# Kernel tuning notes

Measured on AMD Instinct MI355X. Metric: run time of the kernel, lower is better.

Reference implementation:

```python
import jax, jax.numpy as jnp
import numpy as np
import math

H, C, PQ, PV = 12, 16, 4, 8  # heads, head dim, query points, value points
C_S, C_Z = 384, 128
W_C = math.sqrt(2.0 / (9.0 * PQ))
W_L = math.sqrt(1.0 / 3.0)


def setup_inputs() -> dict:
    key = jax.random.key(0)
    ks = jax.random.split(key, 14)
    B, N = 1, 768
    s = jax.random.normal(ks[0], (B, N, C_S), dtype=jnp.float32)
    z = jax.random.normal(ks[1], (B, N, N, C_Z), dtype=jnp.float32)
    R = jax.random.normal(ks[2], (B, N, 3, 3), dtype=jnp.float32)
    t = jax.random.normal(ks[3], (B, N, 3), dtype=jnp.float32)

    def lin(k, fan_in, fan_out):
        return jax.random.normal(k, (fan_in, fan_out), dtype=jnp.float32) / math.sqrt(fan_in)

    out_in = H * C + H * PV * 3 + H * C_Z  # 2016
    return {
        "single_representation": s,
        "pair_representation": z,
        "rotations": R,
        "translation": t,
        "W_q": lin(ks[4], C_S, H * C),
        "W_k": lin(ks[5], C_S, H * C),
        "W_v": lin(ks[6], C_S, H * C),
        "W_qp": lin(ks[7], C_S, 3 * H * PQ),
        "W_kp": lin(ks[8], C_S, 3 * H * PQ),
        "W_vp": lin(ks[9], C_S, 3 * H * PV),
        "W_b": lin(ks[10], C_Z, H),
        "W_out": lin(ks[11], out_in, C_S),
        "b_out": jnp.zeros((C_S,), dtype=jnp.float32),
    }


def reference(single_representation, pair_representation, rotations, translation,
              W_q, W_k, W_v, W_qp, W_kp, W_vp, W_b, W_out, b_out):
    s, z, R, t = single_representation, pair_representation, rotations, translation
    B, N, _ = s.shape

    # scalar q/k/v: [B,N,H,C]
    q = (s @ W_q).reshape(B, N, H, C)
    k = (s @ W_k).reshape(B, N, H, C)
    v = (s @ W_v).reshape(B, N, H, C)

    # local points -> global frames: x_glob = R x_loc + t
    def to_global(pts_flat, P):
        pts = pts_flat.reshape(B, N, H, P, 3)
        return jnp.einsum('bnij,bnhpj->bnhpi', R, pts) + t[:, :, None, None, :]

    q_pts = to_global(s @ W_qp, PQ)  # [B,N,H,PQ,3]
    k_pts = to_global(s @ W_kp, PQ)
    v_pts = to_global(s @ W_vp, PV)  # [B,N,H,PV,3]

    # scalar attention term
    qk = jnp.einsum('bnhc,bmhc->bhnm', q, k) / math.sqrt(C)
    # pair bias term
    bias = jnp.einsum('bnmz,zh->bhnm', z, W_b)
    # point distance term: sum_p ||q_i - k_j||^2 expanded to avoid [N,N,H,P,3]
    qn = jnp.sum(q_pts * q_pts, axis=(-2, -1))  # [B,N,H]
    kn = jnp.sum(k_pts * k_pts, axis=(-2, -1))
    cross = jnp.einsum('bnhpx,bmhpx->bhnm', q_pts, k_pts)
    sq_dist = qn.transpose(0, 2, 1)[:, :, :, None] + kn.transpose(0, 2, 1)[:, :, None, :] - 2.0 * cross

    logits = W_L * (qk + bias - 0.5 * W_C * sq_dist)  # [B,H,N,M]
    a = jax.nn.softmax(logits, axis=-1)

    # outputs
    o = jnp.einsum('bhnm,bmhc->bnhc', a, v).reshape(B, N, H * C)
    o_pts_g = jnp.einsum('bhnm,bmhpx->bnhpx', a, v_pts)
    # inverse frame: R^T (x - t)
    o_pts = jnp.einsum('bnij,bnhpi->bnhpj', R, o_pts_g - t[:, :, None, None, :])
    o_pts = o_pts.reshape(B, N, H * PV * 3)
    o_pair = jnp.einsum('bhnm,bnmz->bnhz', a, z).reshape(B, N, H * C_Z)

    cat = jnp.concatenate([o, o_pts, o_pair], axis=-1)  # [B,N,2016]
    return cat @ W_out + b_out  # [B,N,c_s]
```

## Files before the change

kernel.cpp:

```cpp
#include <hip/hip_runtime.h>
#include <math.h>

#define RAW_OFF   0u
#define QPTS_OFF  884736u
#define KPTS_OFF  995328u
#define VPTS_OFF  1105920u
#define QN_OFF    1327104u
#define KN_OFF    1336320u
#define CAT_OFF   1345536u
#define QP_OFF    2893824u
#define KP_OFF    3041280u
#define SLOG_OFF  3188736u
#define PART2_OFF 10266624u
#define WT_OFF    14118912u

#define WL 0.5773502691896258f
#define WC 0.23570226039551587f
#define CKN (-0.5f*WL*WC)

typedef __attribute__((ext_vector_type(8))) short short8;
typedef __attribute__((ext_vector_type(4))) float f32x4;

__device__ __forceinline__ unsigned short f2bf1(float a) {
  unsigned u = __builtin_bit_cast(unsigned, a);
  return (unsigned short)((u + 0x7fff + ((u >> 16) & 1)) >> 16);
}
__device__ __forceinline__ unsigned f2bf2(float a, float b) {
  unsigned ua = __builtin_bit_cast(unsigned, a), ub = __builtin_bit_cast(unsigned, b);
  return (unsigned)((ua + 0x7fff + ((ua >> 16) & 1)) >> 16)
       | ((ub + 0x7fff + ((ub >> 16) & 1)) & 0xffff0000u);
}
__device__ __forceinline__ float bf2f(unsigned short u) {
  return __builtin_bit_cast(float, ((unsigned)u) << 16);
}

#define BAR_LDS() asm volatile("s_waitcnt lgkmcnt(0)\n\ts_barrier" ::: "memory")

__global__ __launch_bounds__(256) void wcvt(
    const float* __restrict__ Wout, unsigned short* __restrict__ WT)
{
  __shared__ float tl[32][33];
  int b = blockIdx.x;
  int kt = b % 63, ct = b / 63;
  int k0 = kt*32, c0 = ct*32;
  int tr = threadIdx.x >> 5, tc = threadIdx.x & 31;
  #pragma unroll
  for (int i = 0; i < 4; ++i)
    tl[tr + i*8][tc] = Wout[(size_t)(k0 + tr + i*8)*384 + c0 + tc];
  __syncthreads();
  #pragma unroll
  for (int i = 0; i < 4; ++i) {
    int c = tr + i*8;
    WT[(size_t)(c0 + c)*2016 + k0 + tc] = f2bf1(tl[tc][c]);
  }
}

__global__ __launch_bounds__(256) void prep_gemm(
    const float* __restrict__ s, const float* __restrict__ Wq, const float* __restrict__ Wk,
    const float* __restrict__ Wv, const float* __restrict__ Wqp, const float* __restrict__ Wkp,
    const float* __restrict__ Wvp, float* __restrict__ raw)
{
  int t = threadIdx.x;
  int bc = blockIdx.x % 24, br = blockIdx.x / 24;
  int row0 = br * 32, cb = bc * 48;
  const float* W; int outdim, c0;
  if (cb < 192)      { W = Wq;  outdim = 192; c0 = cb; }
  else if (cb < 384) { W = Wk;  outdim = 192; c0 = cb - 192; }
  else if (cb < 576) { W = Wv;  outdim = 192; c0 = cb - 384; }
  else if (cb < 720) { W = Wqp; outdim = 144; c0 = cb - 576; }
  else if (cb < 864) { W = Wkp; outdim = 144; c0 = cb - 720; }
  else               { W = Wvp; outdim = 288; c0 = cb - 864; }

  __shared__ float s_l[32*33];
  __shared__ float w_l[32*49];
  float acc[2][3] = {};
  int tr = t >> 4, tc = t & 15;

  for (int k0 = 0; k0 < 384; k0 += 32) {
    #pragma unroll
    for (int i = 0; i < 4; ++i) {
      int idx = i*256 + t, r = idx >> 5, kk = idx & 31;
      s_l[r*33 + kk] = s[(row0 + r)*384 + k0 + kk];
    }
    #pragma unroll
    for (int i = 0; i < 6; ++i) {
      int idx = i*256 + t, kk = idx / 48, c = idx % 48;
      w_l[kk*49 + c] = W[(k0 + kk)*outdim + c0 + c];
    }
    __syncthreads();
    #pragma unroll
    for (int kk = 0; kk < 32; ++kk) {
      float a0 = s_l[(tr*2+0)*33 + kk], a1 = s_l[(tr*2+1)*33 + kk];
      float b0 = w_l[kk*49 + tc*3 + 0], b1 = w_l[kk*49 + tc*3 + 1], b2 = w_l[kk*49 + tc*3 + 2];
      acc[0][0] += a0*b0; acc[0][1] += a0*b1; acc[0][2] += a0*b2;
      acc[1][0] += a1*b0; acc[1][1] += a1*b1; acc[1][2] += a1*b2;
    }
    __syncthreads();
  }
  #pragma unroll
  for (int i = 0; i < 2; ++i)
    #pragma unroll
    for (int j = 0; j < 3; ++j)
      raw[(row0 + tr*2 + i)*1152 + cb + tc*3 + j] = acc[i][j];
}

__global__ __launch_bounds__(256) void transform_pts(
    const float* __restrict__ raw, const float* __restrict__ R, const float* __restrict__ tg,
    float* __restrict__ qpts, float* __restrict__ kpts, float* __restrict__ vpts,
    float* __restrict__ qn, float* __restrict__ kn)
{
  int n = blockIdx.x, t = threadIdx.x;
  __shared__ float tl[576];
  const float* R9 = R + n*9;
  const float* tv = tg + n*3;
  for (int i = 0; i < 3; ++i) {
    int j = i*256 + t;
    if (j >= 576) break;
    int jj, basecol; float* dst; int dstoff;
    if (j < 144)      { jj = j;      basecol = 576; dst = qpts; dstoff = n*144 + jj; }
    else if (j < 288) { jj = j-144;  basecol = 720; dst = kpts; dstoff = n*144 + jj; }
    else              { jj = j-288;  basecol = 864; dst = vpts; dstoff = n*288 + jj; }
    int x = jj % 3;
    const float* p = raw + n*1152 + basecol + (jj - x);
    float val = R9[x*3+0]*p[0] + R9[x*3+1]*p[1] + R9[x*3+2]*p[2] + tv[x];
    dst[dstoff] = val;
    tl[j] = val;
  }
  __syncthreads();
  if (t < 24) {
    int side = t / 12, h = t % 12;
    const float* q = tl + side*144 + h*12;
    float sm = 0.f;
    #pragma unroll
    for (int r = 0; r < 12; ++r) sm += q[r]*q[r];
    (side == 0 ? qn : kn)[n*12 + h] = sm;
  }
}

__global__ __launch_bounds__(384) void qkprep(
    const float* __restrict__ raw, const float* __restrict__ qpts,
    const float* __restrict__ kpts, short* __restrict__ Qp, short* __restrict__ Kp)
{
  int n = blockIdx.x, t = threadIdx.x;
  int h = t >> 5, k = t & 31;
  float qv, kv;
  if (k < 16)      { qv = (WL*0.25f) * raw[n*1152 + h*16 + k];       kv = raw[n*1152 + 192 + h*16 + k]; }
  else if (k < 28) { qv = (WL*WC) * qpts[n*144 + h*12 + (k-16)];     kv = kpts[n*144 + h*12 + (k-16)]; }
  else             { qv = 0.f; kv = 0.f; }
  Qp[n*384 + t] = (short)f2bf1(qv);
  Kp[n*384 + t] = (short)f2bf1(kv);
}

__global__ __launch_bounds__(512) void logits_gemm(
    const short* __restrict__ Qp, const short* __restrict__ Kp,
    const float* __restrict__ kn, float* __restrict__ slog)
{
  int t = threadIdx.x, b = blockIdx.x;
  int bn = b / 12, bm = b % 12;
  int lane = t & 63, wid = t >> 6;
  int nsub = wid & 3, msub = wid >> 2;
  int l15 = lane & 15, kg = lane >> 4;
  int nrow = bn*64 + nsub*16 + l15;
  int mbase = bm*64 + msub*32;

  f32x4 acc[2][12];
  #pragma unroll
  for (int mt = 0; mt < 2; ++mt)
    #pragma unroll
    for (int h = 0; h < 12; ++h) acc[mt][h] = (f32x4){0.f,0.f,0.f,0.f};

  #pragma unroll
  for (int h = 0; h < 12; ++h) {
    short8 af = *(const short8*)(Qp + (size_t)(nrow*12 + h)*32 + kg*8);
    #pragma unroll
    for (int mt = 0; mt < 2; ++mt) {
      int m = mbase + mt*16 + l15;
      short8 bf = *(const short8*)(Kp + (size_t)(m*12 + h)*32 + kg*8);
      acc[mt][h] = __builtin_amdgcn_mfma_f32_16x16x32_bf16(af, bf, acc[mt][h], 0, 0, 0);
    }
  }
  #pragma unroll
  for (int mt = 0; mt < 2; ++mt) {
    int m = mbase + mt*16 + l15;
    float knadj[12];
    #pragma unroll
    for (int h = 0; h < 12; ++h) knadj[h] = CKN * kn[m*12 + h];
    #pragma unroll
    for (int r = 0; r < 4; ++r) {
      int nr = bn*64 + nsub*16 + kg*4 + r;
      size_t base = ((size_t)nr*768 + m)*12;
      #pragma unroll
      for (int hq = 0; hq < 3; ++hq) {
        float4 v;
        v.x = acc[mt][hq*4+0][r] + knadj[hq*4+0];
        v.y = acc[mt][hq*4+1][r] + knadj[hq*4+1];
        v.z = acc[mt][hq*4+2][r] + knadj[hq*4+2];
        v.w = acc[mt][hq*4+3][r] + knadj[hq*4+3];
        *(float4*)(slog + base + hq*4) = v;
      }
    }
  }
}

#define Z_L   0
#define BIASL 4352
#define PT    5440
#define S_L   6016
#define SMEMW 6028

__global__ __launch_bounds__(256, 2) void ipa_main(
    const float* __restrict__ z, const float* __restrict__ raw,
    const float* __restrict__ slog, const float* __restrict__ vpts,
    const float* __restrict__ Wb, float* __restrict__ part2)
{
  __shared__ __align__(16) unsigned smem[SMEMW];
  float* smf = (float*)smem;
  unsigned short* lds16 = (unsigned short*)smem;
  int bx = blockIdx.x;
  int n = bx >> 1, hb = bx & 1;
  int t = threadIdx.x;
  int lane = t & 63, wid = t >> 6;
  int l15 = lane & 15, kg = lane >> 4;

  if (t < 12) smf[S_L + t] = 0.f;

  short8 wbf[4];
  {
    #pragma unroll
    for (int ks = 0; ks < 4; ++ks)
      #pragma unroll
      for (int e = 0; e < 8; ++e) {
        int kk = ks*32 + kg*8 + e;
        float v = (l15 < 12) ? WL * Wb[kk*12 + l15] : 0.f;
        wbf[ks][e] = (short)f2bf1(v);
      }
  }

  f32x4 oacc[2];
  oacc[0] = (f32x4){0.f,0.f,0.f,0.f};
  oacc[1] = (f32x4){0.f,0.f,0.f,0.f};

  bool dact = t < 240;
  int mh = t / 120, slot = t % 120;
  const float* dsrc; int dstride, dh;
  if (slot < 48) { dh = slot >> 2;     dsrc = raw + 384 + slot*4;  dstride = 1152; }
  else           { dh = (slot-48) / 6; dsrc = vpts + (slot-48)*4;  dstride = 288;  }
  float da0 = 0.f, da1 = 0.f, da2 = 0.f, da3 = 0.f;

  const float* zrow = z + (size_t)n*768*128;
  int ssm = t >> 5, ssc = t & 31;

  float4 zst[8];
  #define STAGE_LOAD(M0)                                                     \
    _Pragma("unroll")                                                        \
    for (int i = 0; i < 8; ++i)                                              \
      zst[i] = *(const float4*)(zrow + (size_t)((M0) + i*8 + ssm)*128 + ssc*4);
  #define STAGE_WRITE()                                                      \
    _Pragma("unroll")                                                        \
    for (int i = 0; i < 8; ++i) {                                            \
      unsigned w0 = f2bf2(zst[i].x, zst[i].y);                               \
      unsigned w1 = f2bf2(zst[i].z, zst[i].w);                               \
      uint2 uu; uu.x = w0; uu.y = w1;                                        \
      *(uint2*)&smem[Z_L + (i*8 + ssm)*68 + ssc*2] = uu;                     \
    }

  const size_t slb = (size_t)n * 9216 + (size_t)hb * 4608;
  float4 sl, slnext;

  STAGE_LOAD(hb*384);
  if (t < 192) sl = *(const float4*)(slog + slb + t*4);
  STAGE_WRITE();
  BAR_LDS();

  for (int it = 0; it < 6; ++it) {
    int m0 = hb*384 + it*64;
    if (it < 5) {
      STAGE_LOAD(m0 + 64);
      if (t < 192) slnext = *(const float4*)(slog + slb + (size_t)(it+1)*768 + t*4);
    }

    {
      f32x4 bacc = (f32x4){0.f,0.f,0.f,0.f};
      int zbase = (wid*16 + l15)*68;
      #pragma unroll
      for (int ks = 0; ks < 4; ++ks) {
        short8 za = *(const short8*)&smem[Z_L + zbase + kg*4 + ks*16];
        bacc = __builtin_amdgcn_mfma_f32_16x16x32_bf16(za, wbf[ks], bacc, 0, 0, 0);
      }
      #pragma unroll
      for (int r = 0; r < 4; ++r)
        smf[BIASL + (wid*16 + kg*4 + r)*17 + l15] = bacc[r];
    }
    BAR_LDS();

    if (t < 192) {
      float slv[4] = {sl.x, sl.y, sl.z, sl.w};
      #pragma unroll
      for (int e = 0; e < 4; ++e) {
        int ge = t*4 + e;
        int m = ge / 12, h = ge - m*12;
        float p = __expf(slv[e] + smf[BIASL + m*17 + h]);
        lds16[PT*2 + h*72 + m] = f2bf1(p);
      }
    }
    BAR_LDS();

    if (t < 48) {
      int h = t >> 2, seg = t & 3;
      short8 a0 = *(const short8*)&lds16[PT*2 + h*72 + seg*16];
      short8 a1 = *(const short8*)&lds16[PT*2 + h*72 + seg*16 + 8];
      float ps = 0.f;
      #pragma unroll
      for (int e = 0; e < 8; ++e)
        ps += bf2f((unsigned short)a0[e]) + bf2f((unsigned short)a1[e]);
      ps += __shfl_xor(ps, 1);
      ps += __shfl_xor(ps, 2);
      if (seg == 0) smf[S_L + h] += ps;
    }

    {
      short8 af[2];
      #pragma unroll
      for (int ks = 0; ks < 2; ++ks)
        af[ks] = *(const short8*)&lds16[PT*2 + l15*72 + ks*32 + kg*8];
      #pragma unroll
      for (int tt = 0; tt < 2; ++tt) {
        int zc = (wid*2 + tt)*16 + l15;
        #pragma unroll
        for (int ks = 0; ks < 2; ++ks) {
          short8 bf;
          #pragma unroll
          for (int e = 0; e < 8; ++e)
            bf[e] = (short)lds16[Z_L*2 + (ks*32 + kg*8 + e)*136 + zc];
          oacc[tt] = __builtin_amdgcn_mfma_f32_16x16x32_bf16(af[ks], bf, oacc[tt], 0, 0, 0);
        }
      }
    }

    if (dact) {
      #pragma unroll
      for (int j4 = 0; j4 < 4; ++j4) {
        short8 pw = *(const short8*)&lds16[PT*2 + dh*72 + mh*32 + j4*8];
        #pragma unroll
        for (int e = 0; e < 8; ++e) {
          float wq = bf2f((unsigned short)pw[e]);
          int row = m0 + mh*32 + j4*8 + e;
          float4 v = *(const float4*)(dsrc + (size_t)row*dstride);
          da0 += wq*v.x; da1 += wq*v.y; da2 += wq*v.z; da3 += wq*v.w;
        }
      }
    }

    if (it < 5) {
      BAR_LDS();
      STAGE_WRITE();
      if (t < 192) sl = slnext;
    }
    BAR_LDS();
  }

  float* pb = part2 + (size_t)bx * 2508;
  if (t < 12) pb[t] = smf[S_L + t];
  if (dact) {
    float4 dv; dv.x = da0; dv.y = da1; dv.z = da2; dv.w = da3;
    *(float4*)(pb + 12 + (mh*120 + slot)*4) = dv;
  }
  if (kg < 3) {
    #pragma unroll
    for (int tt = 0; tt < 2; ++tt) {
      int zc = (wid*2 + tt)*16 + l15;
      #pragma unroll
      for (int r = 0; r < 4; ++r)
        pb[972 + (kg*4 + r)*128 + zc] = oacc[tt][r];
    }
  }
}

__global__ __launch_bounds__(256) void combine(
    const float* __restrict__ part2, const float* __restrict__ Rg,
    const float* __restrict__ tg, unsigned short* __restrict__ catb)
{
  int n = blockIdx.x, t = threadIdx.x;
  const float* b0 = part2 + (size_t)n*2*2508;
  const float* b1 = b0 + 2508;
  __shared__ float S[12], ogl[288];
  if (t < 12) S[t] = b0[t] + b1[t];
  __syncthreads();
  unsigned short* cb = catb + (size_t)n*2016;
  for (int i = t; i < 480; i += 256) {
    float v = b0[12+i] + b0[12+480+i] + b1[12+i] + b1[12+480+i];
    int slot = i >> 2;
    int dh = (slot < 48) ? (slot >> 2) : ((slot - 48) / 6);
    float val = v / S[dh];
    if (i < 192) cb[i] = f2bf1(val);
    else         ogl[i - 192] = val;
  }
  __syncthreads();
  const float* R9 = Rg + n*9;
  const float* tv = tg + n*3;
  for (int j = t; j < 288; j += 256) {
    int x = j % 3, base = j - x;
    float g0 = ogl[base+0] - tv[0];
    float g1 = ogl[base+1] - tv[1];
    float g2 = ogl[base+2] - tv[2];
    cb[192 + j] = f2bf1(R9[x]*g0 + R9[3+x]*g1 + R9[6+x]*g2);
  }
  for (int e = t; e < 1536; e += 256) {
    int h = e >> 7;
    cb[480 + e] = f2bf1((b0[972+e] + b1[972+e]) / S[h]);
  }
}

__global__ __launch_bounds__(256) void final_mfma(
    const unsigned short* __restrict__ catb, const unsigned short* __restrict__ WT,
    const float* __restrict__ bout, float* __restrict__ out)
{
  int t = threadIdx.x, b = blockIdx.x;
  int rt = b / 6, ct = b % 6;
  int r0 = rt*64, c0 = ct*64;
  int lane = t & 63, wid = t >> 6;
  int l15 = lane & 15, kg = lane >> 4;

  f32x4 acc[4];
  #pragma unroll
  for (int cs = 0; cs < 4; ++cs) acc[cs] = (f32x4){0.f,0.f,0.f,0.f};

  const unsigned short* arow = catb + (size_t)(r0 + wid*16 + l15)*2016;
  for (int k0 = 0; k0 < 2016; k0 += 32) {
    short8 af = *(const short8*)(arow + k0 + kg*8);
    #pragma unroll
    for (int cs = 0; cs < 4; ++cs) {
      short8 bf = *(const short8*)(WT + (size_t)(c0 + cs*16 + l15)*2016 + k0 + kg*8);
      acc[cs] = __builtin_amdgcn_mfma_f32_16x16x32_bf16(af, bf, acc[cs], 0, 0, 0);
    }
  }
  #pragma unroll
  for (int cs = 0; cs < 4; ++cs) {
    #pragma unroll
    for (int r = 0; r < 4; ++r) {
      int nn = r0 + wid*16 + kg*4 + r;
      int c  = c0 + cs*16 + l15;
      out[(size_t)nn*384 + c] = acc[cs][r] + bout[c];
    }
  }
}

extern "C" void kernel_launch(void* const* d_in, const int* in_sizes, int n_in,
                              void* d_out, int out_size, void* d_ws, size_t ws_size,
                              hipStream_t stream) {
  const float* s    = (const float*)d_in[0];
  const float* z    = (const float*)d_in[1];
  const float* R    = (const float*)d_in[2];
  const float* tv   = (const float*)d_in[3];
  const float* Wq   = (const float*)d_in[4];
  const float* Wk   = (const float*)d_in[5];
  const float* Wv   = (const float*)d_in[6];
  const float* Wqp  = (const float*)d_in[7];
  const float* Wkp  = (const float*)d_in[8];
  const float* Wvp  = (const float*)d_in[9];
  const float* Wb   = (const float*)d_in[10];
  const float* Wout = (const float*)d_in[11];
  const float* bout = (const float*)d_in[12];
  float* out = (float*)d_out;
  float* ws  = (float*)d_ws;

  float* raw  = ws + RAW_OFF;
  float* qpts = ws + QPTS_OFF;
  float* kpts = ws + KPTS_OFF;
  float* vpts = ws + VPTS_OFF;
  float* qn   = ws + QN_OFF;
  float* kn   = ws + KN_OFF;
  unsigned short* catb = (unsigned short*)(ws + CAT_OFF);
  short* Qp   = (short*)(ws + QP_OFF);
  short* Kp   = (short*)(ws + KP_OFF);
  float* slog = ws + SLOG_OFF;
  float* part2 = ws + PART2_OFF;
  unsigned short* WT = (unsigned short*)(ws + WT_OFF);

  wcvt<<<756, 256, 0, stream>>>(Wout, WT);
  prep_gemm<<<576, 256, 0, stream>>>(s, Wq, Wk, Wv, Wqp, Wkp, Wvp, raw);
  transform_pts<<<768, 256, 0, stream>>>(raw, R, tv, qpts, kpts, vpts, qn, kn);
  qkprep<<<768, 384, 0, stream>>>(raw, qpts, kpts, Qp, Kp);
  logits_gemm<<<144, 512, 0, stream>>>(Qp, Kp, kn, slog);
  ipa_main<<<1536, 256, 0, stream>>>(z, raw, slog, vpts, Wb, part2);
  combine<<<768, 256, 0, stream>>>(part2, R, tv, catb);
  final_mfma<<<72, 256, 0, stream>>>(catb, WT, bout, out);
}
```

Before: 220.0 us.

## Use bf16 MFMA for input projections and fuse point transform with QK packing

Replaces the fp32 LDS-tiled projection GEMM with a bf16 MFMA kernel, fed by new kernels that convert s and the concatenated, transposed projection weights to bf16. The point transform and QK packing kernels are merged, so query and key points and qn no longer go through global memory. This targets the cost of the scalar fp32 GEMM and one kernel launch. It adds two conversion launches and lowers the precision of the projections, which also affects v and the value points.

```diff
diff --git a/kernel.cpp b/kernel.cpp
--- a/kernel.cpp
+++ b/kernel.cpp
@@ -1,18 +1,17 @@
 #include <hip/hip_runtime.h>
 #include <math.h>
 
-#define RAW_OFF   0u
-#define QPTS_OFF  884736u
-#define KPTS_OFF  995328u
-#define VPTS_OFF  1105920u
-#define QN_OFF    1327104u
-#define KN_OFF    1336320u
-#define CAT_OFF   1345536u
-#define QP_OFF    2893824u
-#define KP_OFF    3041280u
-#define SLOG_OFF  3188736u
-#define PART2_OFF 10266624u
-#define WT_OFF    14118912u
+#define RAW_OFF    0u
+#define VPTS_OFF   884736u
+#define KN_OFF     1105920u
+#define CAT_OFF    1115136u
+#define QP_OFF     1889280u
+#define KP_OFF     2036736u
+#define SLOG_OFF   2184192u
+#define PART2_OFF  9262080u
+#define WT_OFF     13114368u
+#define SB_OFF     13501440u
+#define WTC_OFF    13648896u
 
 #define WL 0.5773502691896258f
 #define WC 0.23570226039551587f
@@ -35,6 +34,37 @@
 }
 
 #define BAR_LDS() asm volatile("s_waitcnt lgkmcnt(0)\n\ts_barrier" ::: "memory")
+
+__global__ __launch_bounds__(256) void scvt(
+    const float* __restrict__ s, unsigned short* __restrict__ sb)
+{
+  int g = blockIdx.x*256 + threadIdx.x;
+  float4 v = *(const float4*)(s + (size_t)g*4);
+  uint2 p; p.x = f2bf2(v.x, v.y); p.y = f2bf2(v.z, v.w);
+  *(uint2*)(sb + (size_t)g*4) = p;
+}
+
+__global__ __launch_bounds__(256) void wcatcvt(
+    const float* __restrict__ Wq, const float* __restrict__ Wk, const float* __restrict__ Wv,
+    const float* __restrict__ Wqp, const float* __restrict__ Wkp, const float* __restrict__ Wvp,
+    unsigned short* __restrict__ wtc)
+{
+  int g = blockIdx.x*256 + threadIdx.x;
+  int c = g / 96, kq = (g % 96) * 4;
+  const float* W; int od, cl;
+  if (c < 192)      { W = Wq;  od = 192; cl = c; }
+  else if (c < 384) { W = Wk;  od = 192; cl = c - 192; }
+  else if (c < 576) { W = Wv;  od = 192; cl = c - 384; }
+  else if (c < 720) { W = Wqp; od = 144; cl = c - 576; }
+  else if (c < 864) { W = Wkp; od = 144; cl = c - 720; }
+  else              { W = Wvp; od = 288; cl = c - 864; }
+  float a = W[(size_t)(kq+0)*od + cl];
+  float b = W[(size_t)(kq+1)*od + cl];
+  float d = W[(size_t)(kq+2)*od + cl];
+  float e = W[(size_t)(kq+3)*od + cl];
+  uint2 p; p.x = f2bf2(a, b); p.y = f2bf2(d, e);
+  *(uint2*)(wtc + (size_t)c*384 + kq) = p;
+}
 
 __global__ __launch_bounds__(256) void wcvt(
     const float* __restrict__ Wout, unsigned short* __restrict__ WT)
@@ -55,100 +85,78 @@
   }
 }
 
-__global__ __launch_bounds__(256) void prep_gemm(
-    const float* __restrict__ s, const float* __restrict__ Wq, const float* __restrict__ Wk,
-    const float* __restrict__ Wv, const float* __restrict__ Wqp, const float* __restrict__ Wkp,
-    const float* __restrict__ Wvp, float* __restrict__ raw)
-{
-  int t = threadIdx.x;
-  int bc = blockIdx.x % 24, br = blockIdx.x / 24;
-  int row0 = br * 32, cb = bc * 48;
-  const float* W; int outdim, c0;
-  if (cb < 192)      { W = Wq;  outdim = 192; c0 = cb; }
-  else if (cb < 384) { W = Wk;  outdim = 192; c0 = cb - 192; }
-  else if (cb < 576) { W = Wv;  outdim = 192; c0 = cb - 384; }
-  else if (cb < 720) { W = Wqp; outdim = 144; c0 = cb - 576; }
-  else if (cb < 864) { W = Wkp; outdim = 144; c0 = cb - 720; }
-  else               { W = Wvp; outdim = 288; c0 = cb - 864; }
-
-  __shared__ float s_l[32*33];
-  __shared__ float w_l[32*49];
-  float acc[2][3] = {};
-  int tr = t >> 4, tc = t & 15;
+__global__ __launch_bounds__(256) void prep_mfma(
+    const unsigned short* __restrict__ sb, const unsigned short* __restrict__ wtc,
+    float* __restrict__ raw)
+{
+  int t = threadIdx.x, b = blockIdx.x;
+  int ct = b % 18, rt = b / 18;
+  int lane = t & 63, wid = t >> 6;
+  int l15 = lane & 15, kg = lane >> 4;
+  int r0 = rt*64 + wid*16, c0 = ct*64;
+
+  f32x4 acc[4];
+  #pragma unroll
+  for (int cs = 0; cs < 4; ++cs) acc[cs] = (f32x4){0.f,0.f,0.f,0.f};
 
   for (int k0 = 0; k0 < 384; k0 += 32) {
-    #pragma unroll
-    for (int i = 0; i < 4; ++i) {
-      int idx = i*256 + t, r = idx >> 5, kk = idx & 31;
-      s_l[r*33 + kk] = s[(row0 + r)*384 + k0 + kk];
-    }
-    #pragma unroll
-    for (int i = 0; i < 6; ++i) {
-      int idx = i*256 + t, kk = idx / 48, c = idx % 48;
-      w_l[kk*49 + c] = W[(k0 + kk)*outdim + c0 + c];
-    }
-    __syncthreads();
-    #pragma unroll
-    for (int kk = 0; kk < 32; ++kk) {
-      float a0 = s_l[(tr*2+0)*33 + kk], a1 = s_l[(tr*2+1)*33 + kk];
-      float b0 = w_l[kk*49 + tc*3 + 0], b1 = w_l[kk*49 + tc*3 + 1], b2 = w_l[kk*49 + tc*3 + 2];
-      acc[0][0] += a0*b0; acc[0][1] += a0*b1; acc[0][2] += a0*b2;
-      acc[1][0] += a1*b0; acc[1][1] += a1*b1; acc[1][2] += a1*b2;
-    }
-    __syncthreads();
-  }
-  #pragma unroll
-  for (int i = 0; i < 2; ++i)
-    #pragma unroll
-    for (int j = 0; j < 3; ++j)
-      raw[(row0 + tr*2 + i)*1152 + cb + tc*3 + j] = acc[i][j];
-}
-
-__global__ __launch_bounds__(256) void transform_pts(
+    short8 af = *(const short8*)(sb + (size_t)(r0 + l15)*384 + k0 + kg*8);
+    #pragma unroll
+    for (int cs = 0; cs < 4; ++cs) {
+      short8 bf = *(const short8*)(wtc + (size_t)(c0 + cs*16 + l15)*384 + k0 + kg*8);
+      acc[cs] = __builtin_amdgcn_mfma_f32_16x16x32_bf16(af, bf, acc[cs], 0, 0, 0);
+    }
+  }
+  #pragma unroll
+  for (int cs = 0; cs < 4; ++cs)
+    #pragma unroll
+    for (int r = 0; r < 4; ++r)
+      raw[(size_t)(r0 + kg*4 + r)*1152 + c0 + cs*16 + l15] = acc[cs][r];
+}
+
+__global__ __launch_bounds__(256) void transform_qk(
     const float* __restrict__ raw, const float* __restrict__ R, const float* __restrict__ tg,
-    float* __restrict__ qpts, float* __restrict__ kpts, float* __restrict__ vpts,
-    float* __restrict__ qn, float* __restrict__ kn)
+    float* __restrict__ vpts, float* __restrict__ kn,
+    short* __restrict__ Qp, short* __restrict__ Kp)
 {
   int n = blockIdx.x, t = threadIdx.x;
   __shared__ float tl[576];
   const float* R9 = R + n*9;
   const float* tv = tg + n*3;
+  #pragma unroll
   for (int i = 0; i < 3; ++i) {
     int j = i*256 + t;
     if (j >= 576) break;
-    int jj, basecol; float* dst; int dstoff;
-    if (j < 144)      { jj = j;      basecol = 576; dst = qpts; dstoff = n*144 + jj; }
-    else if (j < 288) { jj = j-144;  basecol = 720; dst = kpts; dstoff = n*144 + jj; }
-    else              { jj = j-288;  basecol = 864; dst = vpts; dstoff = n*288 + jj; }
+    int jj, basecol;
+    if (j < 144)      { jj = j;      basecol = 576; }
+    else if (j < 288) { jj = j-144;  basecol = 720; }
+    else              { jj = j-288;  basecol = 864; }
     int x = jj % 3;
     const float* p = raw + n*1152 + basecol + (jj - x);
     float val = R9[x*3+0]*p[0] + R9[x*3+1]*p[1] + R9[x*3+2]*p[2] + tv[x];
-    dst[dstoff] = val;
+    if (j >= 288) vpts[n*288 + jj] = val;
     tl[j] = val;
   }
   __syncthreads();
-  if (t < 24) {
-    int side = t / 12, h = t % 12;
-    const float* q = tl + side*144 + h*12;
+  if (t < 12) {
+    const float* q = tl + 144 + t*12;
     float sm = 0.f;
     #pragma unroll
     for (int r = 0; r < 12; ++r) sm += q[r]*q[r];
-    (side == 0 ? qn : kn)[n*12 + h] = sm;
-  }
-}
-
-__global__ __launch_bounds__(384) void qkprep(
-    const float* __restrict__ raw, const float* __restrict__ qpts,
-    const float* __restrict__ kpts, short* __restrict__ Qp, short* __restrict__ Kp)
-{
-  int n = blockIdx.x, t = threadIdx.x;
-  int h = t >> 5, k = t & 31;
-  float qv, kv;
-  if (k < 16)      { qv = (WL*0.25f) * raw[n*1152 + h*16 + k];       kv = raw[n*1152 + 192 + h*16 + k]; }
-  else if (k < 28) { qv = (WL*WC) * qpts[n*144 + h*12 + (k-16)];     kv = kpts[n*144 + h*12 + (k-16)]; }
-  else             { qv = 0.f; kv = 0.f; }
-  Qp[n*384 + t] = (short)f2bf1(qv);
-  Kp[n*384 + t] = (short)f2bf1(kv);
+    kn[n*12 + t] = sm;
+  }
+  #pragma unroll
+  for (int i = 0; i < 2; ++i) {
+    int idx = i*256 + t;
+    if (idx >= 384) break;
+    int h = idx >> 5, k = idx & 31;
+    float qv, kv;
+    if (k < 16)      { qv = (WL*0.25f) * raw[n*1152 + h*16 + k];  kv = raw[n*1152 + 192 + h*16 + k]; }
+    else if (k < 28) { qv = (WL*WC) * tl[h*12 + (k-16)];          kv = tl[144 + h*12 + (k-16)]; }
+    else             { qv = 0.f; kv = 0.f; }
+    Qp[n*384 + idx] = (short)f2bf1(qv);
+    Kp[n*384 + idx] = (short)f2bf1(kv);
+  }
 }
 
 __global__ __launch_bounds__(512) void logits_gemm(
@@ -465,10 +473,7 @@
   float* ws  = (float*)d_ws;
 
   float* raw  = ws + RAW_OFF;
-  float* qpts = ws + QPTS_OFF;
-  float* kpts = ws + KPTS_OFF;
   float* vpts = ws + VPTS_OFF;
-  float* qn   = ws + QN_OFF;
   float* kn   = ws + KN_OFF;
   unsigned short* catb = (unsigned short*)(ws + CAT_OFF);
   short* Qp   = (short*)(ws + QP_OFF);
@@ -476,11 +481,15 @@
   float* slog = ws + SLOG_OFF;
   float* part2 = ws + PART2_OFF;
   unsigned short* WT = (unsigned short*)(ws + WT_OFF);
-
+  unsigned short* sb = (unsigned short*)(ws + SB_OFF);
+  unsigned short* wtc = (unsigned short*)(ws + WTC_OFF);
+
+  scvt<<<288, 256, 0, stream>>>(s, sb);
+  wcatcvt<<<432, 256, 0, stream>>>(Wq, Wk, Wv, Wqp, Wkp, Wvp, wtc);
   wcvt<<<756, 256, 0, stream>>>(Wout, WT);
-  prep_gemm<<<576, 256, 0, stream>>>(s, Wq, Wk, Wv, Wqp, Wkp, Wvp, raw);
-  transform_pts<<<768, 256, 0, stream>>>(raw, R, tv, qpts, kpts, vpts, qn, kn);
-  qkprep<<<768, 384, 0, stream>>>(raw, qpts, kpts, Qp, Kp);
+
+  prep_mfma<<<216, 256, 0, stream>>>(sb, wtc, raw);
+  transform_qk<<<768, 256, 0, stream>>>(raw, R, tv, vpts, kn, Qp, Kp);
   logits_gemm<<<144, 512, 0, stream>>>(Qp, Kp, kn, slog);
   ipa_main<<<1536, 256, 0, stream>>>(z, raw, slog, vpts, Wb, part2);
   combine<<<768, 256, 0, stream>>>(part2, R, tv, catb);
```

Result: faster. 201.6 us (-8.4%).
